# Optimization experiments

Hardware: AMD Instinct MI355X
Metric: run time of the kernel (lower is better)

Reference implementation:

```python
import jax, jax.numpy as jnp
import numpy as np

NUM_GRAPHS = 64
NUM_LAYERS = 3
HEADS = 4
HID = 64
DMODEL = HEADS * HID  # 256
NUM_EDGE_TYPES = 8
NUM_CLASSES = 2
N_NODES = 30000
N_EDGES = 240000


def setup_inputs() -> dict:
    key = jax.random.key(0)
    ks = jax.random.split(key, 16)
    s = 0.05
    x = jax.random.normal(ks[0], (N_NODES, DMODEL), jnp.float32)
    edge_index = jax.random.randint(ks[1], (2, N_EDGES), 0, N_NODES)
    batch = jnp.sort(jax.random.randint(ks[2], (N_NODES,), 0, NUM_GRAPHS))
    edge_type_ids = jax.random.randint(ks[3], (N_EDGES,), 0, NUM_EDGE_TYPES)
    # stacked per-layer conv params (all layers are DMODEL -> HEADS*HID = DMODEL)
    Wq = jax.random.normal(ks[4], (NUM_LAYERS, DMODEL, DMODEL), jnp.float32) * s
    bq = jax.random.normal(ks[5], (NUM_LAYERS, DMODEL), jnp.float32) * s
    Wk = jax.random.normal(ks[6], (NUM_LAYERS, DMODEL, DMODEL), jnp.float32) * s
    bk = jax.random.normal(ks[7], (NUM_LAYERS, DMODEL), jnp.float32) * s
    Wv = jax.random.normal(ks[8], (NUM_LAYERS, DMODEL, DMODEL), jnp.float32) * s
    bv = jax.random.normal(ks[9], (NUM_LAYERS, DMODEL), jnp.float32) * s
    Eemb = jax.random.normal(ks[10], (NUM_LAYERS, NUM_EDGE_TYPES, DMODEL), jnp.float32) * s
    # 1-layer GRU (PyTorch layout: [3*hid, in], gate order r, z, n)
    W_ih = jax.random.normal(ks[11], (3 * HID, DMODEL), jnp.float32) * s
    b_ih = jax.random.normal(ks[12], (3 * HID,), jnp.float32) * s
    W_hh = jax.random.normal(ks[13], (3 * HID, HID), jnp.float32) * s
    b_hh = jax.random.normal(ks[14], (3 * HID,), jnp.float32) * s
    W_fc = jax.random.normal(ks[15], (NUM_CLASSES, HID), jnp.float32) * s
    b_fc = jnp.zeros((NUM_CLASSES,), jnp.float32)
    return dict(x=x, edge_index=edge_index, batch=batch, edge_type_ids=edge_type_ids,
                Wq=Wq, bq=bq, Wk=Wk, bk=bk, Wv=Wv, bv=bv, Eemb=Eemb,
                W_ih=W_ih, b_ih=b_ih, W_hh=W_hh, b_hh=b_hh, W_fc=W_fc, b_fc=b_fc)


def reference(x, edge_index, batch, edge_type_ids, Wq, bq, Wk, bk, Wv, bv, Eemb,
              W_ih, b_ih, W_hh, b_hh, W_fc, b_fc):
    N = x.shape[0]
    src, dst = edge_index[0], edge_index[1]  # messages flow src -> dst
    scale = 1.0 / jnp.sqrt(jnp.float32(HID))
    for l in range(NUM_LAYERS):
        q = (x @ Wq[l] + bq[l]).reshape(N, HEADS, HID)
        k_all = x @ Wk[l] + bk[l]  # [N, DMODEL]
        v_all = x @ Wv[l] + bv[l]
        ete = Eemb[l][edge_type_ids]  # edge-type conditioning, [E, DMODEL]
        k = (k_all[src] + ete).reshape(-1, HEADS, HID)
        v = (v_all[src] + ete).reshape(-1, HEADS, HID)
        scores = jnp.einsum('ehd,ehd->eh', q[dst], k) * scale  # [E, H]
        # per-destination-node segment softmax (stable)
        m = jax.ops.segment_max(scores, dst, num_segments=N)
        ex = jnp.exp(scores - m[dst])
        den = jax.ops.segment_sum(ex, dst, num_segments=N)
        alpha = ex / (den[dst] + 1e-16)
        agg = jax.ops.segment_sum(alpha[..., None] * v, dst, num_segments=N)
        x = jax.nn.elu(agg.reshape(N, DMODEL))
    # global mean pool over graphs
    cnt = jax.ops.segment_sum(jnp.ones((N,), x.dtype), batch, num_segments=NUM_GRAPHS)
    g = jax.ops.segment_sum(x, batch, num_segments=NUM_GRAPHS) / jnp.maximum(cnt, 1.0)[:, None]
    # single GRU step from h0 = 0 (seq_len == 1)
    h0 = jnp.zeros((NUM_GRAPHS, HID), x.dtype)
    gi = g @ W_ih.T + b_ih
    gh = h0 @ W_hh.T + b_hh
    ir, iz, inn = jnp.split(gi, 3, axis=-1)
    hr, hz, hn = jnp.split(gh, 3, axis=-1)
    r = jax.nn.sigmoid(ir + hr)
    z = jax.nn.sigmoid(iz + hz)
    n = jnp.tanh(inn + r * hn)
    h = (1.0 - z) * n + z * h0
    return h @ W_fc.T + b_fc  # [NUM_GRAPHS, NUM_CLASSES]
```

## Files before the change

kernel.cpp:

```cpp
#include <hip/hip_runtime.h>
#include <math.h>

#define N_NODES 30000
#define N_EDGES 240000
#define DMODEL 256
#define NETYPES 8
#define NGRAPHS 64
#define NLAYERS 3

typedef __attribute__((ext_vector_type(8))) short short8;
typedef __attribute__((ext_vector_type(8))) unsigned short ushort8;
typedef __attribute__((ext_vector_type(4))) float f32x4;

__device__ __forceinline__ unsigned short f2bf(float f) {
  union { float f; unsigned u; } v; v.f = f;
  unsigned r = v.u + 0x7FFF + ((v.u >> 16) & 1);
  return (unsigned short)(r >> 16);
}
__device__ __forceinline__ float bf2f(unsigned short h) {
  union { unsigned u; float f; } v; v.u = ((unsigned)h) << 16;
  return v.f;
}

__device__ __forceinline__ void async_g2l(const unsigned short* g, unsigned short* l) {
  __builtin_amdgcn_global_load_lds(
      (const __attribute__((address_space(1))) void*)g,
      (__attribute__((address_space(3))) void*)l, 16, 0, 0);
}

__device__ __forceinline__ float dpp_red_add(float x) {
  int v = __float_as_int(x);
  int t;
  t = __builtin_amdgcn_update_dpp(0, v, 0xB1, 0xF, 0xF, true);
  v = __float_as_int(__int_as_float(v) + __int_as_float(t));
  t = __builtin_amdgcn_update_dpp(0, v, 0x4E, 0xF, 0xF, true);
  v = __float_as_int(__int_as_float(v) + __int_as_float(t));
  t = __builtin_amdgcn_update_dpp(0, v, 0x141, 0xF, 0xF, true);
  v = __float_as_int(__int_as_float(v) + __int_as_float(t));
  t = __builtin_amdgcn_update_dpp(0, v, 0x140, 0xF, 0xF, true);
  v = __float_as_int(__int_as_float(v) + __int_as_float(t));
  return __int_as_float(v);
}

__global__ void k_count_deg(const int* __restrict__ dst, int* __restrict__ deg) {
  int e = blockIdx.x * blockDim.x + threadIdx.x;
  if (e < N_EDGES) atomicAdd(&deg[dst[e]], 1);
}

__global__ __launch_bounds__(1024) void k_scan(const int* __restrict__ deg,
                                               int* __restrict__ rowstart,
                                               int* __restrict__ cursor) {
  const int C = 30;
  int tid = threadIdx.x;
  int base = tid * C;
  int vals[C];
  int sum = 0;
#pragma unroll
  for (int j = 0; j < C; ++j) {
    int idx = base + j;
    int v = (idx < N_NODES) ? deg[idx] : 0;
    vals[j] = sum;
    sum += v;
  }
  int lane = tid & 63, wv = tid >> 6;
  int s = sum;
#pragma unroll
  for (int off = 1; off < 64; off <<= 1) {
    int t2 = __shfl_up(s, off);
    if (lane >= off) s += t2;
  }
  __shared__ int wsum[16];
  if (lane == 63) wsum[wv] = s;
  __syncthreads();
  if (tid == 0) {
    int a = 0;
#pragma unroll
    for (int i = 0; i < 16; ++i) { int t2 = wsum[i]; wsum[i] = a; a += t2; }
    rowstart[N_NODES] = a;
  }
  __syncthreads();
  int texcl = wsum[wv] + (s - sum);
#pragma unroll
  for (int j = 0; j < C; ++j) {
    int idx = base + j;
    if (idx < N_NODES) {
      int p = texcl + vals[j];
      rowstart[idx] = p;
      cursor[idx]   = p;
    }
  }
}

__global__ void k_scatter(const int* __restrict__ src, const int* __restrict__ dst,
                          const int* __restrict__ etype, int* __restrict__ cursor,
                          int* __restrict__ packed) {
  int e = blockIdx.x * blockDim.x + threadIdx.x;
  if (e < N_EDGES) {
    int p = atomicAdd(&cursor[dst[e]], 1);
    packed[p] = src[e] * NETYPES + etype[e];
  }
}

__global__ __launch_bounds__(256) void k_cvt_w(
    const float* __restrict__ Wq, const float* __restrict__ Wk, const float* __restrict__ Wv,
    unsigned short* __restrict__ wthi) {
  __shared__ float tile[32][33];
  int k0 = blockIdx.x * 32;
  int n0g = blockIdx.y * 32;
  int l = blockIdx.z;
  int which = n0g >> 8;
  int col0 = n0g & 255;
  const float* W = (which == 0) ? Wq : ((which == 1) ? Wk : Wv);
  int c = threadIdx.x & 31, r = threadIdx.x >> 5;
#pragma unroll
  for (int rr = 0; rr < 4; ++rr) {
    int kk = r + rr * 8;
    tile[kk][c] = W[(size_t)l * 65536 + (size_t)(k0 + kk) * 256 + col0 + c];
  }
  __syncthreads();
  int kk = threadIdx.x & 31, nn0 = threadIdx.x >> 5;
#pragma unroll
  for (int rr = 0; rr < 4; ++rr) {
    int nn = nn0 + rr * 8;
    wthi[((size_t)l * 768 + n0g + nn) * 256 + k0 + kk] = f2bf(tile[kk][nn]);
  }
}

__global__ void k_cvt_b(const float* __restrict__ bq, const float* __restrict__ bk,
                        const float* __restrict__ bv, float* __restrict__ bcat) {
  int idx = blockIdx.x * 256 + threadIdx.x;
  if (idx >= NLAYERS * 768) return;
  int n = idx % 768, l = idx / 768;
  int which = n >> 8, col = n & 255;
  const float* b = (which == 0) ? bq : ((which == 1) ? bk : bv);
  bcat[idx] = b[l * 256 + col];
}

__global__ void k_cvt_x(const float* __restrict__ x, unsigned short* __restrict__ xhi,
                        unsigned short* __restrict__ xlo) {
  int i = blockIdx.x * 256 + threadIdx.x;
  if (i < N_NODES * 256) {
    float v = x[i];
    unsigned short h = f2bf(v);
    xhi[i] = h;
    xlo[i] = f2bf(v - bf2f(h));
  }
}

__global__ __launch_bounds__(256) void k_gemm_mfma(
    const unsigned short* __restrict__ Ahi, const unsigned short* __restrict__ Alo,
    const unsigned short* __restrict__ Bhi,
    const float* __restrict__ bcat, float* __restrict__ qbuf,
    unsigned short* __restrict__ kv) {
  __shared__ unsigned short smem[2 * 12288];

  int tid = threadIdx.x;
  int lane = tid & 63, wave = tid >> 6;
  int bx = blockIdx.x;
  int xcd = bx & 7, slot = bx >> 3;
  int rt = xcd + (slot / 6) * 8;
  if (rt >= 235) return;
  int row0 = rt * 128;
  int n0 = (slot % 6) * 128;
  int wm = (wave >> 1) * 64, wn = (wave & 1) * 64;
  int quad = lane >> 4, l16 = lane & 15;
  int chunk = lane & 3;
  int srow = wave * 32 + (lane >> 2);

  f32x4 acc[4][4];
#pragma unroll
  for (int i = 0; i < 4; ++i)
#pragma unroll
    for (int j = 0; j < 4; ++j) acc[i][j] = (f32x4)(0.f);

  auto STAGE = [&](int k0, int b) {
    unsigned short* s = smem + b * 12288;
#pragma unroll
    for (int j = 0; j < 2; ++j) {
      int r = srow + j * 16;
      int ldsoff = wave * 1024 + j * 512;
      int garA = row0 + r; if (garA >= N_NODES) garA = N_NODES - 1;
      size_t aoff = (size_t)garA * 256 + k0 + chunk * 8;
      async_g2l(Ahi + aoff, s + ldsoff);
      async_g2l(Alo + aoff, s + 4096 + ldsoff);
      size_t boff = (size_t)(n0 + r) * 256 + k0 + chunk * 8;
      async_g2l(Bhi + boff, s + 8192 + ldsoff);
    }
  };

  STAGE(0, 0);
#pragma unroll
  for (int k = 0; k < 8; ++k) {
    int cur = k & 1;
    if (k < 7) {
      STAGE((k + 1) * 32, cur ^ 1);
      asm volatile("s_waitcnt vmcnt(6)" ::: "memory");
    } else {
      asm volatile("s_waitcnt vmcnt(0)" ::: "memory");
    }
    __builtin_amdgcn_s_barrier();

    const unsigned short* sAhi = smem + cur * 12288;
    const unsigned short* sAlo = sAhi + 4096;
    const unsigned short* sBhi = sAhi + 8192;
    short8 ah[4], al[4], bh[4];
#pragma unroll
    for (int i = 0; i < 4; ++i) {
      int off = (wm + i * 16 + l16) * 32 + quad * 8;
      ah[i] = *(const short8*)(sAhi + off);
      al[i] = *(const short8*)(sAlo + off);
    }
#pragma unroll
    for (int j = 0; j < 4; ++j) {
      int off = (wn + j * 16 + l16) * 32 + quad * 8;
      bh[j] = *(const short8*)(sBhi + off);
    }
#pragma unroll
    for (int i = 0; i < 4; ++i)
#pragma unroll
      for (int j = 0; j < 4; ++j) {
        acc[i][j] = __builtin_amdgcn_mfma_f32_16x16x32_bf16(ah[i], bh[j], acc[i][j], 0, 0, 0);
        acc[i][j] = __builtin_amdgcn_mfma_f32_16x16x32_bf16(al[i], bh[j], acc[i][j], 0, 0, 0);
      }
    __builtin_amdgcn_s_barrier();
  }

  float bj[4];
#pragma unroll
  for (int j = 0; j < 4; ++j) bj[j] = bcat[n0 + wn + j * 16 + l16];
  bool isq = (n0 < 256);
  int cb = n0 - 256;
  int isV = cb >> 8;
  int cc0 = (cb & 255) + wn + l16;
#pragma unroll
  for (int i = 0; i < 4; ++i) {
    int rowb = row0 + wm + i * 16 + quad * 4;
#pragma unroll
    for (int r = 0; r < 4; ++r) {
      int grow = rowb + r;
      if (grow < N_NODES) {
        if (isq) {
          float* cp = qbuf + (size_t)grow * 256 + n0 + wn + l16;
#pragma unroll
          for (int j = 0; j < 4; ++j) cp[j * 16] = acc[i][j][r] + bj[j];
        } else {
          unsigned short* rowp = kv + (size_t)grow * 512 + isV * 4;
#pragma unroll
          for (int j = 0; j < 4; ++j) {
            int c = cc0 + j * 16;
            rowp[((c >> 2) << 3) + (c & 3)] = f2bf(acc[i][j][r] + bj[j]);
          }
        }
      }
    }
  }
}

__global__ __launch_bounds__(256) void k_attn(
    const float* __restrict__ qbuf, const unsigned short* __restrict__ kv,
    const int* __restrict__ rowstart, const int* __restrict__ packed,
    const float* __restrict__ Eemb_l,
    unsigned short* __restrict__ xhi, unsigned short* __restrict__ xlo) {
  __shared__ float ete_s[NETYPES * 256];
  __shared__ int pk_s[512];
  int t = threadIdx.x;
#pragma unroll
  for (int i = 0; i < NETYPES; ++i) ete_s[i * 256 + t] = Eemb_l[i * 256 + t];
  int nb = blockIdx.x * 4;
  int brs = rowstart[nb], bre = rowstart[nb + 4];
  int cnt = bre - brs;
  if (cnt <= 512) {
    for (int j = t; j < cnt; j += 256) pk_s[j] = packed[brs + j];
  }
  __syncthreads();
  int lane = t & 63;
  int n = nb + (t >> 6);
  float4 q4 = ((const float4*)(qbuf + (size_t)n * 256))[lane];
  int rs = rowstart[n], re = rowstart[n + 1];
  float l1 = 0.f, ax1 = 0.f, ay1 = 0.f, az1 = 0.f, aw1 = 0.f;
  float l2 = 0.f, ax2 = 0.f, ay2 = 0.f, az2 = 0.f, aw2 = 0.f;

  if (cnt <= 512) {
    int i = rs - brs, ie = re - brs;
    for (; i + 2 <= ie; i += 2) {
      int pkA = pk_s[i], pkB = pk_s[i + 1];
      const unsigned short* baseA = kv + (size_t)(pkA >> 3) * 512;
      const unsigned short* baseB = kv + (size_t)(pkB >> 3) * 512;
      ushort8 cA = ((const ushort8*)baseA)[lane];
      ushort8 cB = ((const ushort8*)baseB)[lane];
      float4 eA = ((const float4*)(ete_s + (pkA & 7) * 256))[lane];
      float4 eB = ((const float4*)(ete_s + (pkB & 7) * 256))[lane];
      float pA = (bf2f(cA[0]) + eA.x) * q4.x + (bf2f(cA[1]) + eA.y) * q4.y +
                 (bf2f(cA[2]) + eA.z) * q4.z + (bf2f(cA[3]) + eA.w) * q4.w;
      float pB = (bf2f(cB[0]) + eB.x) * q4.x + (bf2f(cB[1]) + eB.y) * q4.y +
                 (bf2f(cB[2]) + eB.z) * q4.z + (bf2f(cB[3]) + eB.w) * q4.w;
      pA = dpp_red_add(pA);
      pB = dpp_red_add(pB);
      float e1 = __expf(pA * 0.125f);
      float e2 = __expf(pB * 0.125f);
      l1 += e1; l2 += e2;
      ax1 = fmaf(e1, bf2f(cA[4]) + eA.x, ax1);
      ay1 = fmaf(e1, bf2f(cA[5]) + eA.y, ay1);
      az1 = fmaf(e1, bf2f(cA[6]) + eA.z, az1);
      aw1 = fmaf(e1, bf2f(cA[7]) + eA.w, aw1);
      ax2 = fmaf(e2, bf2f(cB[4]) + eB.x, ax2);
      ay2 = fmaf(e2, bf2f(cB[5]) + eB.y, ay2);
      az2 = fmaf(e2, bf2f(cB[6]) + eB.z, az2);
      aw2 = fmaf(e2, bf2f(cB[7]) + eB.w, aw2);
    }
    if (i < ie) {
      int pk = pk_s[i];
      const unsigned short* base = kv + (size_t)(pk >> 3) * 512;
      ushort8 cA = ((const ushort8*)base)[lane];
      float4 e4 = ((const float4*)(ete_s + (pk & 7) * 256))[lane];
      float p = (bf2f(cA[0]) + e4.x) * q4.x + (bf2f(cA[1]) + e4.y) * q4.y +
                (bf2f(cA[2]) + e4.z) * q4.z + (bf2f(cA[3]) + e4.w) * q4.w;
      p = dpp_red_add(p);
      float e1 = __expf(p * 0.125f);
      l1 += e1;
      ax1 = fmaf(e1, bf2f(cA[4]) + e4.x, ax1);
      ay1 = fmaf(e1, bf2f(cA[5]) + e4.y, ay1);
      az1 = fmaf(e1, bf2f(cA[6]) + e4.z, az1);
      aw1 = fmaf(e1, bf2f(cA[7]) + e4.w, aw1);
    }
  } else {
    for (int i = rs; i < re; ++i) {
      int pk = packed[i];
      const unsigned short* base = kv + (size_t)(pk >> 3) * 512;
      ushort8 cA = ((const ushort8*)base)[lane];
      float4 e4 = ((const float4*)(ete_s + (pk & 7) * 256))[lane];
      float p = (bf2f(cA[0]) + e4.x) * q4.x + (bf2f(cA[1]) + e4.y) * q4.y +
                (bf2f(cA[2]) + e4.z) * q4.z + (bf2f(cA[3]) + e4.w) * q4.w;
      p = dpp_red_add(p);
      float e1 = __expf(p * 0.125f);
      l1 += e1;
      ax1 = fmaf(e1, bf2f(cA[4]) + e4.x, ax1);
      ay1 = fmaf(e1, bf2f(cA[5]) + e4.y, ay1);
      az1 = fmaf(e1, bf2f(cA[6]) + e4.z, az1);
      aw1 = fmaf(e1, bf2f(cA[7]) + e4.w, aw1);
    }
  }

  float l = l1 + l2;
  float inv = 1.f / (l + 1e-16f);
  float4 o;
  o.x = (ax1 + ax2) * inv; o.y = (ay1 + ay2) * inv;
  o.z = (az1 + az2) * inv; o.w = (aw1 + aw2) * inv;
  o.x = o.x > 0.f ? o.x : expm1f(o.x);
  o.y = o.y > 0.f ? o.y : expm1f(o.y);
  o.z = o.z > 0.f ? o.z : expm1f(o.z);
  o.w = o.w > 0.f ? o.w : expm1f(o.w);
  unsigned short h0 = f2bf(o.x), h1 = f2bf(o.y), h2 = f2bf(o.z), h3 = f2bf(o.w);
  ushort4 hv, lv;
  hv.x = h0; hv.y = h1; hv.z = h2; hv.w = h3;
  lv.x = f2bf(o.x - bf2f(h0)); lv.y = f2bf(o.y - bf2f(h1));
  lv.z = f2bf(o.z - bf2f(h2)); lv.w = f2bf(o.w - bf2f(h3));
  size_t base_o = (size_t)n * 256 + lane * 4;
  *(ushort4*)(xhi + base_o) = hv;
  *(ushort4*)(xlo + base_o) = lv;
}

__global__ __launch_bounds__(256) void k_pool_partial(
    const unsigned short* __restrict__ xhi, const unsigned short* __restrict__ xlo,
    const int* __restrict__ batch, float* __restrict__ gacc) {
  int t = threadIdx.x;
  int base = blockIdx.x * 128;
  int end = base + 128; if (end > N_NODES) end = N_NODES;
  __shared__ int bsh[128];
  if (t < 128 && base + t < N_NODES) bsh[t] = batch[base + t];
  __syncthreads();
  float acc = 0.f;
  int cur = bsh[0];
  for (int n = base; n < end; ++n) {
    int g = bsh[n - base];
    if (g != cur) {
      atomicAdd(&gacc[cur * 256 + t], acc);
      acc = 0.f; cur = g;
    }
    size_t idx = (size_t)n * 256 + t;
    acc += bf2f(xhi[idx]) + bf2f(xlo[idx]);
  }
  atomicAdd(&gacc[cur * 256 + t], acc);
}

__device__ inline int lower_bound_dev(const int* a, int n, int val) {
  int lo = 0, hi = n;
  while (lo < hi) {
    int mid = (lo + hi) >> 1;
    if (a[mid] < val) lo = mid + 1; else hi = mid;
  }
  return lo;
}

__global__ __launch_bounds__(256) void k_gru_fc(
    const float* __restrict__ gacc, const int* __restrict__ batch,
    const float* __restrict__ W_ih, const float* __restrict__ b_ih,
    const float* __restrict__ b_hh, const float* __restrict__ W_fc,
    const float* __restrict__ b_fc, float* __restrict__ out) {
  __shared__ float gv[256];
  __shared__ float gates[192];
  __shared__ float h[64];
  int gr = blockIdx.x, t = threadIdx.x;
  int s0 = lower_bound_dev(batch, N_NODES, gr);
  int e0 = lower_bound_dev(batch, N_NODES, gr + 1);
  float c = (e0 > s0) ? (float)(e0 - s0) : 1.f;
  gv[t] = gacc[gr * 256 + t] / c;
  __syncthreads();
  if (t < 192) {
    const float* wr = W_ih + t * 256;
    float s = b_ih[t];
    for (int k = 0; k < 256; ++k) s = fmaf(gv[k], wr[k], s);
    gates[t] = s;
  }
  __syncthreads();
  if (t < 64) {
    float r  = 1.f / (1.f + expf(-(gates[t] + b_hh[t])));
    float z  = 1.f / (1.f + expf(-(gates[64 + t] + b_hh[64 + t])));
    float nn = tanhf(gates[128 + t] + r * b_hh[128 + t]);
    h[t] = (1.f - z) * nn;
  }
  __syncthreads();
  if (t < 2) {
    const float* wr = W_fc + t * 64;
    float s = b_fc[t];
    for (int k = 0; k < 64; ++k) s = fmaf(h[k], wr[k], s);
    out[gr * 2 + t] = s;
  }
}

extern "C" void kernel_launch(void* const* d_in, const int* in_sizes, int n_in,
                              void* d_out, int out_size, void* d_ws, size_t ws_size,
                              hipStream_t stream) {
  const float* x     = (const float*)d_in[0];
  const int* edge_index = (const int*)d_in[1];
  const int* batch   = (const int*)d_in[2];
  const int* etype   = (const int*)d_in[3];
  const float* Wq    = (const float*)d_in[4];
  const float* bq    = (const float*)d_in[5];
  const float* Wk    = (const float*)d_in[6];
  const float* bk    = (const float*)d_in[7];
  const float* Wv    = (const float*)d_in[8];
  const float* bv    = (const float*)d_in[9];
  const float* Eemb  = (const float*)d_in[10];
  const float* W_ih  = (const float*)d_in[11];
  const float* b_ih  = (const float*)d_in[12];
  const float* b_hh  = (const float*)d_in[14];
  const float* W_fc  = (const float*)d_in[15];
  const float* b_fc  = (const float*)d_in[16];
  float* out = (float*)d_out;

  const int* src = edge_index;
  const int* dst = edge_index + N_EDGES;

  float* qbuf  = (float*)d_ws;
  float* gacc  = qbuf + (size_t)N_NODES * 256;
  float* bcat  = gacc + NGRAPHS * 256;
  unsigned short* kv   = (unsigned short*)(bcat + NLAYERS * 768);
  unsigned short* xhi  = kv + (size_t)N_NODES * 512;
  unsigned short* xlo  = xhi + (size_t)N_NODES * 256;
  unsigned short* wthi = xlo + (size_t)N_NODES * 256;
  int* deg      = (int*)(wthi + (size_t)NLAYERS * 768 * 256);
  int* rowstart = deg + N_NODES;
  int* cursor   = rowstart + N_NODES + 1;
  int* packed   = cursor + N_NODES;

  hipMemsetAsync(deg, 0, N_NODES * sizeof(int), stream);
  hipMemsetAsync(gacc, 0, NGRAPHS * 256 * sizeof(float), stream);
  k_count_deg<<<(N_EDGES + 255) / 256, 256, 0, stream>>>(dst, deg);
  k_scan<<<1, 1024, 0, stream>>>(deg, rowstart, cursor);
  k_scatter<<<(N_EDGES + 255) / 256, 256, 0, stream>>>(src, dst, etype, cursor, packed);

  k_cvt_w<<<dim3(8, 24, 3), 256, 0, stream>>>(Wq, Wk, Wv, wthi);
  k_cvt_b<<<(NLAYERS * 768 + 255) / 256, 256, 0, stream>>>(bq, bk, bv, bcat);
  k_cvt_x<<<(N_NODES * 256 + 255) / 256, 256, 0, stream>>>(x, xhi, xlo);

  for (int l = 0; l < NLAYERS; ++l) {
    k_gemm_mfma<<<1440, 256, 0, stream>>>(
        xhi, xlo, wthi + (size_t)l * 768 * 256,
        bcat + l * 768, qbuf, kv);
    k_attn<<<N_NODES / 4, 256, 0, stream>>>(qbuf, kv, rowstart, packed,
                                            Eemb + (size_t)l * NETYPES * 256, xhi, xlo);
  }
  k_pool_partial<<<(N_NODES + 127) / 128, 256, 0, stream>>>(xhi, xlo, batch, gacc);
  k_gru_fc<<<NGRAPHS, 256, 0, stream>>>(gacc, batch, W_ih, b_ih, b_hh, W_fc, b_fc, out);
}
```

Measured before the change: 454.8 us.

## Shrink GEMM row tile, swizzle LDS, and software-pipeline attention edge gathers

The MFMA projection GEMM drops from 128-row to 64-row tiles, which doubles the grid, shrinks LDS per block, and requests 5 blocks per CU through launch bounds. It also XOR-swizzles the LDS chunk layout to avoid bank conflicts. The attention kernel now prefetches the next pair of K/V rows before processing the current pair, double-buffered in registers, to hide gather latency. The costs are more reloads of B per output row, higher register pressure in the attention loop, and a single accumulator chain in place of the previous two.

```diff
diff --git a/kernel.cpp b/kernel.cpp
--- a/kernel.cpp
+++ b/kernel.cpp
@@ -147,44 +147,44 @@
   }
 }
 
-__global__ __launch_bounds__(256) void k_gemm_mfma(
+__global__ __launch_bounds__(256, 5) void k_gemm_mfma(
     const unsigned short* __restrict__ Ahi, const unsigned short* __restrict__ Alo,
     const unsigned short* __restrict__ Bhi,
     const float* __restrict__ bcat, float* __restrict__ qbuf,
     unsigned short* __restrict__ kv) {
-  __shared__ unsigned short smem[2 * 12288];
+  __shared__ unsigned short smem[2 * 8192];
 
   int tid = threadIdx.x;
   int lane = tid & 63, wave = tid >> 6;
   int bx = blockIdx.x;
   int xcd = bx & 7, slot = bx >> 3;
   int rt = xcd + (slot / 6) * 8;
-  if (rt >= 235) return;
-  int row0 = rt * 128;
+  if (rt >= 469) return;
+  int row0 = rt * 64;
   int n0 = (slot % 6) * 128;
-  int wm = (wave >> 1) * 64, wn = (wave & 1) * 64;
+  int wm = (wave >> 1) * 32, wn = (wave & 1) * 64;
   int quad = lane >> 4, l16 = lane & 15;
-  int chunk = lane & 3;
-  int srow = wave * 32 + (lane >> 2);
-
-  f32x4 acc[4][4];
-#pragma unroll
-  for (int i = 0; i < 4; ++i)
+  int lrow = lane >> 2;
+  int chSw = (lane & 3) ^ ((lane >> 3) & 3);
+  int rdSw = (quad ^ ((l16 >> 1) & 3)) * 8;
+
+  f32x4 acc[2][4];
+#pragma unroll
+  for (int i = 0; i < 2; ++i)
 #pragma unroll
     for (int j = 0; j < 4; ++j) acc[i][j] = (f32x4)(0.f);
 
   auto STAGE = [&](int k0, int b) {
-    unsigned short* s = smem + b * 12288;
-#pragma unroll
-    for (int j = 0; j < 2; ++j) {
-      int r = srow + j * 16;
-      int ldsoff = wave * 1024 + j * 512;
-      int garA = row0 + r; if (garA >= N_NODES) garA = N_NODES - 1;
-      size_t aoff = (size_t)garA * 256 + k0 + chunk * 8;
-      async_g2l(Ahi + aoff, s + ldsoff);
-      async_g2l(Alo + aoff, s + 4096 + ldsoff);
-      size_t boff = (size_t)(n0 + r) * 256 + k0 + chunk * 8;
-      async_g2l(Bhi + boff, s + 8192 + ldsoff);
+    unsigned short* s = smem + b * 8192;
+    int garA = row0 + wave * 16 + lrow; if (garA >= N_NODES) garA = N_NODES - 1;
+    size_t acol = (size_t)garA * 256 + k0 + chSw * 8;
+    async_g2l(Ahi + acol, s + wave * 512);
+    async_g2l(Alo + acol, s + 2048 + wave * 512);
+#pragma unroll
+    for (int r = 0; r < 2; ++r) {
+      int brow = r * 64 + wave * 16 + lrow;
+      size_t boff = (size_t)(n0 + brow) * 256 + k0 + chSw * 8;
+      async_g2l(Bhi + boff, s + 4096 + r * 2048 + wave * 512);
     }
   };
 
@@ -194,29 +194,29 @@
     int cur = k & 1;
     if (k < 7) {
       STAGE((k + 1) * 32, cur ^ 1);
-      asm volatile("s_waitcnt vmcnt(6)" ::: "memory");
+      asm volatile("s_waitcnt vmcnt(4)" ::: "memory");
     } else {
       asm volatile("s_waitcnt vmcnt(0)" ::: "memory");
     }
     __builtin_amdgcn_s_barrier();
 
-    const unsigned short* sAhi = smem + cur * 12288;
-    const unsigned short* sAlo = sAhi + 4096;
-    const unsigned short* sBhi = sAhi + 8192;
-    short8 ah[4], al[4], bh[4];
-#pragma unroll
-    for (int i = 0; i < 4; ++i) {
-      int off = (wm + i * 16 + l16) * 32 + quad * 8;
+    const unsigned short* sAhi = smem + cur * 8192;
+    const unsigned short* sAlo = sAhi + 2048;
+    const unsigned short* sB   = sAhi + 4096;
+    short8 ah[2], al[2], bh[4];
+#pragma unroll
+    for (int i = 0; i < 2; ++i) {
+      int off = (wm + i * 16 + l16) * 32 + rdSw;
       ah[i] = *(const short8*)(sAhi + off);
       al[i] = *(const short8*)(sAlo + off);
     }
 #pragma unroll
     for (int j = 0; j < 4; ++j) {
-      int off = (wn + j * 16 + l16) * 32 + quad * 8;
-      bh[j] = *(const short8*)(sBhi + off);
-    }
-#pragma unroll
-    for (int i = 0; i < 4; ++i)
+      int off = (wn + j * 16 + l16) * 32 + rdSw;
+      bh[j] = *(const short8*)(sB + off);
+    }
+#pragma unroll
+    for (int i = 0; i < 2; ++i)
 #pragma unroll
       for (int j = 0; j < 4; ++j) {
         acc[i][j] = __builtin_amdgcn_mfma_f32_16x16x32_bf16(ah[i], bh[j], acc[i][j], 0, 0, 0);
@@ -233,7 +233,7 @@
   int isV = cb >> 8;
   int cc0 = (cb & 255) + wn + l16;
 #pragma unroll
-  for (int i = 0; i < 4; ++i) {
+  for (int i = 0; i < 2; ++i) {
     int rowb = row0 + wm + i * 16 + quad * 4;
 #pragma unroll
     for (int r = 0; r < 4; ++r) {
@@ -255,6 +255,20 @@
     }
   }
 }
+
+#define GATHER(PK) (((const ushort8*)(kv + (size_t)((PK) >> 3) * 512))[lane])
+
+#define PROC(PK, C)                                                      \
+  { float4 e4 = ((const float4*)(ete_s + ((PK) & 7) * 256))[lane];       \
+    float p_ = (bf2f(C[0]) + e4.x) * q4.x + (bf2f(C[1]) + e4.y) * q4.y + \
+               (bf2f(C[2]) + e4.z) * q4.z + (bf2f(C[3]) + e4.w) * q4.w;  \
+    p_ = dpp_red_add(p_);                                                \
+    float e1_ = __expf(p_ * 0.125f);                                     \
+    lsum += e1_;                                                         \
+    ax = fmaf(e1_, bf2f(C[4]) + e4.x, ax);                               \
+    ay = fmaf(e1_, bf2f(C[5]) + e4.y, ay);                               \
+    az = fmaf(e1_, bf2f(C[6]) + e4.z, az);                               \
+    aw = fmaf(e1_, bf2f(C[7]) + e4.w, aw); }
 
 __global__ __launch_bounds__(256) void k_attn(
     const float* __restrict__ qbuf, const unsigned short* __restrict__ kv,
@@ -277,75 +291,51 @@
   int n = nb + (t >> 6);
   float4 q4 = ((const float4*)(qbuf + (size_t)n * 256))[lane];
   int rs = rowstart[n], re = rowstart[n + 1];
-  float l1 = 0.f, ax1 = 0.f, ay1 = 0.f, az1 = 0.f, aw1 = 0.f;
-  float l2 = 0.f, ax2 = 0.f, ay2 = 0.f, az2 = 0.f, aw2 = 0.f;
+  float lsum = 0.f, ax = 0.f, ay = 0.f, az = 0.f, aw = 0.f;
 
   if (cnt <= 512) {
-    int i = rs - brs, ie = re - brs;
-    for (; i + 2 <= ie; i += 2) {
-      int pkA = pk_s[i], pkB = pk_s[i + 1];
-      const unsigned short* baseA = kv + (size_t)(pkA >> 3) * 512;
-      const unsigned short* baseB = kv + (size_t)(pkB >> 3) * 512;
-      ushort8 cA = ((const ushort8*)baseA)[lane];
-      ushort8 cB = ((const ushort8*)baseB)[lane];
-      float4 eA = ((const float4*)(ete_s + (pkA & 7) * 256))[lane];
-      float4 eB = ((const float4*)(ete_s + (pkB & 7) * 256))[lane];
-      float pA = (bf2f(cA[0]) + eA.x) * q4.x + (bf2f(cA[1]) + eA.y) * q4.y +
-                 (bf2f(cA[2]) + eA.z) * q4.z + (bf2f(cA[3]) + eA.w) * q4.w;
-      float pB = (bf2f(cB[0]) + eB.x) * q4.x + (bf2f(cB[1]) + eB.y) * q4.y +
-                 (bf2f(cB[2]) + eB.z) * q4.z + (bf2f(cB[3]) + eB.w) * q4.w;
-      pA = dpp_red_add(pA);
-      pB = dpp_red_add(pB);
-      float e1 = __expf(pA * 0.125f);
-      float e2 = __expf(pB * 0.125f);
-      l1 += e1; l2 += e2;
-      ax1 = fmaf(e1, bf2f(cA[4]) + eA.x, ax1);
-      ay1 = fmaf(e1, bf2f(cA[5]) + eA.y, ay1);
-      az1 = fmaf(e1, bf2f(cA[6]) + eA.z, az1);
-      aw1 = fmaf(e1, bf2f(cA[7]) + eA.w, aw1);
-      ax2 = fmaf(e2, bf2f(cB[4]) + eB.x, ax2);
-      ay2 = fmaf(e2, bf2f(cB[5]) + eB.y, ay2);
-      az2 = fmaf(e2, bf2f(cB[6]) + eB.z, az2);
-      aw2 = fmaf(e2, bf2f(cB[7]) + eB.w, aw2);
-    }
-    if (i < ie) {
-      int pk = pk_s[i];
-      const unsigned short* base = kv + (size_t)(pk >> 3) * 512;
-      ushort8 cA = ((const ushort8*)base)[lane];
-      float4 e4 = ((const float4*)(ete_s + (pk & 7) * 256))[lane];
-      float p = (bf2f(cA[0]) + e4.x) * q4.x + (bf2f(cA[1]) + e4.y) * q4.y +
-                (bf2f(cA[2]) + e4.z) * q4.z + (bf2f(cA[3]) + e4.w) * q4.w;
-      p = dpp_red_add(p);
-      float e1 = __expf(p * 0.125f);
-      l1 += e1;
-      ax1 = fmaf(e1, bf2f(cA[4]) + e4.x, ax1);
-      ay1 = fmaf(e1, bf2f(cA[5]) + e4.y, ay1);
-      az1 = fmaf(e1, bf2f(cA[6]) + e4.z, az1);
-      aw1 = fmaf(e1, bf2f(cA[7]) + e4.w, aw1);
+    int i0 = rs - brs, ie = re - brs;
+    int m = ie - i0;
+    int npair = m >> 1;
+    int pkA0 = 0, pkB0 = 0, pkA1 = 0, pkB1 = 0;
+    ushort8 cA0 = (ushort8)(unsigned short)0, cB0 = cA0, cA1 = cA0, cB1 = cA0;
+    if (npair >= 1) {
+      pkA0 = pk_s[i0]; pkB0 = pk_s[i0 + 1];
+      cA0 = GATHER(pkA0); cB0 = GATHER(pkB0);
+    }
+    for (int p = 0; p < npair; ++p) {
+      int nx = i0 + 2 * p + 2;
+      if ((p & 1) == 0) {
+        if (p + 1 < npair) {
+          pkA1 = pk_s[nx]; pkB1 = pk_s[nx + 1];
+          cA1 = GATHER(pkA1); cB1 = GATHER(pkB1);
+        }
+        PROC(pkA0, cA0) PROC(pkB0, cB0)
+      } else {
+        if (p + 1 < npair) {
+          pkA0 = pk_s[nx]; pkB0 = pk_s[nx + 1];
+          cA0 = GATHER(pkA0); cB0 = GATHER(pkB0);
+        }
+        PROC(pkA1, cA1) PROC(pkB1, cB1)
+      }
+    }
+    if (m & 1) {
+      int pk = pk_s[ie - 1];
+      ushort8 c = GATHER(pk);
+      PROC(pk, c)
     }
   } else {
     for (int i = rs; i < re; ++i) {
       int pk = packed[i];
-      const unsigned short* base = kv + (size_t)(pk >> 3) * 512;
-      ushort8 cA = ((const ushort8*)base)[lane];
-      float4 e4 = ((const float4*)(ete_s + (pk & 7) * 256))[lane];
-      float p = (bf2f(cA[0]) + e4.x) * q4.x + (bf2f(cA[1]) + e4.y) * q4.y +
-                (bf2f(cA[2]) + e4.z) * q4.z + (bf2f(cA[3]) + e4.w) * q4.w;
-      p = dpp_red_add(p);
-      float e1 = __expf(p * 0.125f);
-      l1 += e1;
-      ax1 = fmaf(e1, bf2f(cA[4]) + e4.x, ax1);
-      ay1 = fmaf(e1, bf2f(cA[5]) + e4.y, ay1);
-      az1 = fmaf(e1, bf2f(cA[6]) + e4.z, az1);
-      aw1 = fmaf(e1, bf2f(cA[7]) + e4.w, aw1);
-    }
-  }
-
-  float l = l1 + l2;
-  float inv = 1.f / (l + 1e-16f);
+      ushort8 c = GATHER(pk);
+      PROC(pk, c)
+    }
+  }
+
+  float inv = 1.f / (lsum + 1e-16f);
   float4 o;
-  o.x = (ax1 + ax2) * inv; o.y = (ay1 + ay2) * inv;
-  o.z = (az1 + az2) * inv; o.w = (aw1 + aw2) * inv;
+  o.x = ax * inv; o.y = ay * inv;
+  o.z = az * inv; o.w = aw * inv;
   o.x = o.x > 0.f ? o.x : expm1f(o.x);
   o.y = o.y > 0.f ? o.y : expm1f(o.y);
   o.z = o.z > 0.f ? o.z : expm1f(o.z);
@@ -475,7 +465,7 @@
   k_cvt_x<<<(N_NODES * 256 + 255) / 256, 256, 0, stream>>>(x, xhi, xlo);
 
   for (int l = 0; l < NLAYERS; ++l) {
-    k_gemm_mfma<<<1440, 256, 0, stream>>>(
+    k_gemm_mfma<<<59 * 8 * 6, 256, 0, stream>>>(
         xhi, xlo, wthi + (size_t)l * 768 * 256,
         bcat + l * 768, qbuf, kv);
     k_attn<<<N_NODES / 4, 256, 0, stream>>>(qbuf, kv, rowstart, packed,
```

Result: no change. 460.3 us (+1.2%).
